# Kernel tuning notes

Hardware: AMD Instinct MI355X
Metric: run time of the kernel (lower is better)

Reference implementation:

```python
import jax, jax.numpy as jnp
import numpy as np

L, B, H, P = 2048, 32, 128, 256  # seq len, batch, feature dim, state dim


def setup_inputs() -> dict:
    key = jax.random.key(0)
    ks = jax.random.split(key, 9)
    log_min, log_max = np.log(0.001), np.log(0.1)
    return {
        "input_sequences": jax.random.normal(ks[0], (L, B, H), dtype=jnp.float32),
        # -Lambda.real of a HiPPO block diag is positive; emulate with small positive values
        "log_Lambda_real": jnp.log(0.5 + jax.random.uniform(ks[1], (P,), dtype=jnp.float32)),
        "Lambda_imag": jax.random.normal(ks[2], (P,), dtype=jnp.float32) * 3.0,
        "B_tilde_r": jax.random.normal(ks[3], (P, H), dtype=jnp.float32) * (0.5 / np.sqrt(H)),
        "B_tilde_i": jax.random.normal(ks[4], (P, H), dtype=jnp.float32) * (0.5 / np.sqrt(H)),
        "C_tilde_r": jax.random.normal(ks[5], (H, P), dtype=jnp.float32) * (0.5 / np.sqrt(P)),
        "C_tilde_i": jax.random.normal(ks[6], (H, P), dtype=jnp.float32) * (0.5 / np.sqrt(P)),
        "D": jax.random.normal(ks[7], (H,), dtype=jnp.float32),
        "log_Delta": log_min + (log_max - log_min) * jax.random.uniform(ks[8], (P,), dtype=jnp.float32),
    }


def reference(input_sequences, log_Lambda_real, Lambda_imag, B_tilde_r, B_tilde_i,
              C_tilde_r, C_tilde_i, D, log_Delta):
    l = input_sequences.shape[0]
    u = input_sequences.astype(jnp.complex64)  # (L,B,H)
    lam = (-jnp.exp(log_Lambda_real) + 1j * Lambda_imag).astype(jnp.complex64)  # (P,)
    log_Lambda_bar = lam * jnp.exp(log_Delta).astype(jnp.complex64)  # scale_factor=1.0
    # kernel[t, p] = exp(log_Lambda_bar[p] * (L-1-t))  -> (L,P)
    steps = jnp.arange(l - 1, -1, -1, dtype=jnp.float32).astype(jnp.complex64)
    kernel = jnp.exp(steps[:, None] * log_Lambda_bar[None, :])
    B_tilde = (B_tilde_r + 1j * B_tilde_i).astype(jnp.complex64)  # (P,H)
    B_bar = ((kernel[-2] - 1.0) / lam)[:, None] * B_tilde  # (P,H)
    Bu = jnp.einsum('nm,lbm->lbn', B_bar, u)  # (L,B,P)
    # FFT convolution: flipped kernel is exp(log_Lambda_bar * t)
    kff = jnp.fft.fft(kernel[::-1], n=2 * l, axis=0)[:, None, :]  # (2L,1,P)
    buff = jnp.fft.fft(Bu, n=2 * l, axis=0)  # (2L,B,P)
    o = jnp.fft.ifft(kff * buff, axis=0)[:l]  # (L,B,P)
    xs = jnp.einsum('hn,lbn->lbh', (C_tilde_r + 1j * C_tilde_i).astype(jnp.complex64), o)
    xs = xs + (D * input_sequences).astype(jnp.complex64)
    return jnp.real(xs)
```

## Files before the change

### kernel.cpp

```cpp
#include <hip/hip_runtime.h>
#include <math.h>

#define SL 2048
#define NB 32
#define NH 128
#define NP 256
#define NP2 512

typedef short bf16x8 __attribute__((ext_vector_type(8)));
typedef float f32x4  __attribute__((ext_vector_type(4)));

static __device__ __forceinline__ unsigned short f2bf(float x) {
    unsigned u = __float_as_uint(x);
    return (unsigned short)((u + 0x7fffu + ((u >> 16) & 1u)) >> 16);
}
static __device__ __forceinline__ float bf2f(unsigned short h) {
    return __uint_as_float(((unsigned)h) << 16);
}
static __device__ __forceinline__ void discretize(
    const float* __restrict__ logLr, const float* __restrict__ Lim,
    const float* __restrict__ logDt, int p, float& wr, float& wi)
{
    const float Lr = expf(logLr[p]);
    const float dt = expf(logDt[p]);
    const float ew = expf(-Lr * dt);
    const float ang = Lim[p] * dt;
    wr = ew * cosf(ang); wi = ew * sinf(ang);
}

__global__ __launch_bounds__(256) void k0(
    const float* __restrict__ logLr, const float* __restrict__ Lim,
    const float* __restrict__ logDt,
    const float* __restrict__ Br, const float* __restrict__ Bi,
    const float* __restrict__ Cr, const float* __restrict__ Ci,
    unsigned short* __restrict__ Bhat, unsigned short* __restrict__ Chat)
{
    const int tid = blockIdx.x * 256 + threadIdx.x;
    const int p = tid >> 7, h = tid & 127;
    float wr, wi; discretize(logLr, Lim, logDt, p, wr, wi);
    const float Lr = expf(logLr[p]), li = Lim[p];
    const float nr = wr - 1.0f, ni = wi;
    const float den = Lr * Lr + li * li;
    const float fr = (-nr * Lr + ni * li) / den;
    const float fi = (-ni * Lr - nr * li) / den;
    const float br = Br[p * NH + h], bi = Bi[p * NH + h];
    Bhat[(size_t)(2 * p)     * NH + h] = f2bf(fr * br - fi * bi);
    Bhat[(size_t)(2 * p + 1) * NH + h] = f2bf(fr * bi + fi * br);
    Chat[(size_t)h * NP2 + 2 * p]     = f2bf(Cr[h * NP + p]);
    Chat[(size_t)h * NP2 + 2 * p + 1] = f2bf(-Ci[h * NP + p]);
}

__global__ __launch_bounds__(256, 2) void gA(
    const float* __restrict__ u, const unsigned short* __restrict__ Bhat,
    const float* __restrict__ logLr, const float* __restrict__ Lim,
    const float* __restrict__ logDt,
    unsigned short* __restrict__ bu, float2* __restrict__ part)
{
    __shared__ unsigned short us[32][136];
    __shared__ unsigned xs[32 * 257];

    const int seg = blockIdx.x;
    const int b   = blockIdx.y;
    const int tid = threadIdx.x;
    const int wave = tid >> 6, lane = tid & 63;
    const int q = lane >> 4, c = lane & 15;
    const int pbase = wave * 128;

    bf16x8 A[4][8];
    #pragma unroll
    for (int kk = 0; kk < 4; ++kk)
        #pragma unroll
        for (int mt = 0; mt < 8; ++mt)
            A[kk][mt] = *(const bf16x8*)(Bhat + (size_t)(pbase + 16 * mt + c) * NH
                                              + kk * 32 + 8 * q);

    float wr, wi; discretize(logLr, Lim, logDt, tid, wr, wi);
    float W32r = wr, W32i = wi;
    #pragma unroll
    for (int t = 0; t < 5; ++t) { const float r = W32r * W32r - W32i * W32i;
                                  W32i = 2.f * W32r * W32i; W32r = r; }

    float2 pa = make_float2(0.f, 0.f);

    for (int t = 0; t < 4; ++t) {
        const int l0 = seg * 128 + t * 32;
        __syncthreads();
        {
            const int lrow = tid >> 3;
            const int hcol = (tid & 7) * 16;
            const float* up = u + (size_t)(l0 + lrow) * (NB * NH) + b * NH + hcol;
            float4 a = *(const float4*)(up + 0);
            float4 d = *(const float4*)(up + 4);
            float4 e = *(const float4*)(up + 8);
            float4 g = *(const float4*)(up + 12);
            uint4 w0, w1;
            w0.x = (unsigned)f2bf(a.x) | ((unsigned)f2bf(a.y) << 16);
            w0.y = (unsigned)f2bf(a.z) | ((unsigned)f2bf(a.w) << 16);
            w0.z = (unsigned)f2bf(d.x) | ((unsigned)f2bf(d.y) << 16);
            w0.w = (unsigned)f2bf(d.z) | ((unsigned)f2bf(d.w) << 16);
            w1.x = (unsigned)f2bf(e.x) | ((unsigned)f2bf(e.y) << 16);
            w1.y = (unsigned)f2bf(e.z) | ((unsigned)f2bf(e.w) << 16);
            w1.z = (unsigned)f2bf(g.x) | ((unsigned)f2bf(g.y) << 16);
            w1.w = (unsigned)f2bf(g.z) | ((unsigned)f2bf(g.w) << 16);
            *(uint4*)&us[lrow][hcol + 0] = w0;
            *(uint4*)&us[lrow][hcol + 8] = w1;
        }
        __syncthreads();

        f32x4 acc[8][2];
        #pragma unroll
        for (int mt = 0; mt < 8; ++mt)
            #pragma unroll
            for (int nt = 0; nt < 2; ++nt) acc[mt][nt] = (f32x4){0.f, 0.f, 0.f, 0.f};

        #pragma unroll
        for (int kk = 0; kk < 4; ++kk) {
            bf16x8 bfr[2];
            #pragma unroll
            for (int nt = 0; nt < 2; ++nt)
                bfr[nt] = *(const bf16x8*)&us[16 * nt + c][kk * 32 + 8 * q];
            #pragma unroll
            for (int mt = 0; mt < 8; ++mt)
                #pragma unroll
                for (int nt = 0; nt < 2; ++nt)
                    acc[mt][nt] = __builtin_amdgcn_mfma_f32_16x16x32_bf16(
                        A[kk][mt], bfr[nt], acc[mt][nt], 0, 0, 0);
        }

        #pragma unroll
        for (int mt = 0; mt < 8; ++mt)
            #pragma unroll
            for (int nt = 0; nt < 2; ++nt) {
                const int rw = 16 * nt + c;
                const int pp = pbase + 16 * mt + 4 * q;
                ushort4 st;
                st.x = f2bf(acc[mt][nt][0]); st.y = f2bf(acc[mt][nt][1]);
                st.z = f2bf(acc[mt][nt][2]); st.w = f2bf(acc[mt][nt][3]);
                *(ushort4*)(bu + ((size_t)(b * SL + l0 + rw)) * NP2 + pp) = st;
                const int col = (pp >> 1);
                xs[rw * 257 + col]     = (unsigned)st.x | ((unsigned)st.y << 16);
                xs[rw * 257 + col + 1] = (unsigned)st.z | ((unsigned)st.w << 16);
            }
        __syncthreads();

        {
            float sr = 0.f, si = 0.f;
            unsigned va[8], vb[8];
            #pragma unroll
            for (int j = 0; j < 8; ++j) va[j] = xs[j * 257 + tid];
            #pragma unroll
            for (int k8 = 0; k8 < 4; ++k8) {
                if (k8 < 3) {
                    #pragma unroll
                    for (int j = 0; j < 8; ++j) vb[j] = xs[((k8 + 1) * 8 + j) * 257 + tid];
                }
                #pragma unroll
                for (int j = 0; j < 8; ++j) {
                    const float xr = bf2f((unsigned short)(va[j] & 0xffffu));
                    const float xi = bf2f((unsigned short)(va[j] >> 16));
                    const float tr = wr * sr - wi * si + xr;
                    const float ti = wr * si + wi * sr + xi;
                    sr = tr; si = ti;
                }
                #pragma unroll
                for (int j = 0; j < 8; ++j) va[j] = vb[j];
            }
            if ((t & 1) == 0) {
                pa = make_float2(sr, si);
            } else {
                const float cr2 = W32r * pa.x - W32i * pa.y + sr;
                const float ci2 = W32r * pa.y + W32i * pa.x + si;
                part[((size_t)b * 32 + 2 * seg + (t >> 1)) * NP + tid] =
                    make_float2(cr2, ci2);
            }
        }
    }
}

__global__ __launch_bounds__(256) void s2(
    const float2* __restrict__ part, const float* __restrict__ logLr,
    const float* __restrict__ Lim, const float* __restrict__ logDt,
    float2* __restrict__ C)
{
    const int b = blockIdx.x, p = threadIdx.x;
    float wr, wi; discretize(logLr, Lim, logDt, p, wr, wi);
    float Wr = wr, Wi = wi;
    #pragma unroll
    for (int t = 0; t < 6; ++t) { const float r = Wr * Wr - Wi * Wi; Wi = 2.f * Wr * Wi; Wr = r; }
    float sr = 0.f, si = 0.f;
    for (int m = 0; m < 32; ++m) {
        C[(size_t)(b * 32 + m) * NP + p] = make_float2(sr, si);
        const float2 v = part[(size_t)(b * 32 + m) * NP + p];
        const float tr = Wr * sr - Wi * si + v.x;
        const float ti = Wr * si + Wi * sr + v.y;
        sr = tr; si = ti;
    }
}

__global__ __launch_bounds__(256, 2) void gB(
    const unsigned* __restrict__ bu32, const unsigned short* __restrict__ Chat,
    const float* __restrict__ logLr, const float* __restrict__ Lim,
    const float* __restrict__ logDt, const float2* __restrict__ C,
    const float* __restrict__ Dv, const float* __restrict__ u,
    float* __restrict__ out)
{
    __shared__ uint4 os4[4096];
    char*   osb  = (char*)os4;
    float2* carr = (float2*)os4;

    const int m = blockIdx.x, b = blockIdx.y;
    const int tid = threadIdx.x;
    const int w = tid >> 6, lane = tid & 63;
    const int p0 = lane * 4;

    float wr[4], wi[4];
    #pragma unroll
    for (int e = 0; e < 4; ++e) discretize(logLr, Lim, logDt, p0 + e, wr[e], wi[e]);

    float Wr[4], Wi[4];
    #pragma unroll
    for (int e = 0; e < 4; ++e) { Wr[e] = wr[e]; Wi[e] = wi[e]; }
    #pragma unroll
    for (int t = 0; t < 4; ++t)
        #pragma unroll
        for (int e = 0; e < 4; ++e) {
            const float r = Wr[e] * Wr[e] - Wi[e] * Wi[e];
            Wi[e] = 2.f * Wr[e] * Wi[e]; Wr[e] = r;
        }

    const unsigned* base = bu32 + ((size_t)(b * SL + m * 64 + w * 16)) * NP + p0;
    uint4 va[16];
    #pragma unroll
    for (int k = 0; k < 16; ++k) va[k] = *(const uint4*)(base + (size_t)k * NP);

    float sr[4] = {0.f, 0.f, 0.f, 0.f}, si[4] = {0.f, 0.f, 0.f, 0.f};
    #pragma unroll
    for (int k = 0; k < 16; ++k) {
        unsigned vv[4] = { va[k].x, va[k].y, va[k].z, va[k].w };
        #pragma unroll
        for (int e = 0; e < 4; ++e) {
            const float xr = bf2f((unsigned short)(vv[e] & 0xffffu));
            const float xi = bf2f((unsigned short)(vv[e] >> 16));
            const float tr = wr[e] * sr[e] - wi[e] * si[e] + xr;
            const float ti = wr[e] * si[e] + wi[e] * sr[e] + xi;
            sr[e] = tr; si[e] = ti;
        }
    }
    #pragma unroll
    for (int e = 0; e < 4; ++e) carr[w * NP + p0 + e] = make_float2(sr[e], si[e]);

    float Er[4], Ei[4];
    #pragma unroll
    for (int e = 0; e < 4; ++e) {
        const float2 E = C[((size_t)(b * 32 + m)) * NP + p0 + e];
        Er[e] = E.x; Ei[e] = E.y;
    }

    __syncthreads();
    float cjr[3][4], cji[3][4];
    #pragma unroll
    for (int j = 0; j < 3; ++j) if (j < w)
        #pragma unroll
        for (int e = 0; e < 4; ++e) {
            const float2 v = carr[j * NP + p0 + e];
            cjr[j][e] = v.x; cji[j][e] = v.y;
        }
    __syncthreads();

    #pragma unroll
    for (int j = 0; j < 3; ++j) if (j < w)
        #pragma unroll
        for (int e = 0; e < 4; ++e) {
            const float tr = Wr[e] * Er[e] - Wi[e] * Ei[e] + cjr[j][e];
            const float ti = Wr[e] * Ei[e] + Wi[e] * Er[e] + cji[j][e];
            Er[e] = tr; Ei[e] = ti;
        }

    #pragma unroll
    for (int e = 0; e < 4; ++e) { sr[e] = Er[e]; si[e] = Ei[e]; }
    #pragma unroll
    for (int k = 0; k < 16; ++k) {
        unsigned vv[4] = { va[k].x, va[k].y, va[k].z, va[k].w };
        unsigned ov[4];
        #pragma unroll
        for (int e = 0; e < 4; ++e) {
            const float xr = bf2f((unsigned short)(vv[e] & 0xffffu));
            const float xi = bf2f((unsigned short)(vv[e] >> 16));
            const float tr = wr[e] * sr[e] - wi[e] * si[e] + xr;
            const float ti = wr[e] * si[e] + wi[e] * sr[e] + xi;
            sr[e] = tr; si[e] = ti;
            ov[e] = (unsigned)f2bf(tr) | ((unsigned)f2bf(ti) << 16);
        }
        const int row = w * 16 + k;
        const unsigned byte = (((unsigned)row << 10) + ((unsigned)lane << 4))
                              ^ (((unsigned)(k & 7)) << 4);
        uint4 st = { ov[0], ov[1], ov[2], ov[3] };
        *(uint4*)(osb + byte) = st;
    }
    __syncthreads();

    const int q = lane >> 4, c = lane & 15;
    const int wm = w >> 1, wn = w & 1;
    const int hbase = wm * 64;
    const int lbase = m * 64 + wn * 32;

    f32x4 acc[4][2];
    #pragma unroll
    for (int mt = 0; mt < 4; ++mt)
        #pragma unroll
        for (int nt = 0; nt < 2; ++nt) acc[mt][nt] = (f32x4){0.f, 0.f, 0.f, 0.f};

    #pragma unroll 4
    for (int kk = 0; kk < 16; ++kk) {
        bf16x8 af[4];
        #pragma unroll
        for (int mt = 0; mt < 4; ++mt)
            af[mt] = *(const bf16x8*)(Chat + (size_t)(hbase + 16 * mt + c) * NP2
                                           + kk * 32 + 8 * q);
        bf16x8 bfr[2];
        #pragma unroll
        for (int nt = 0; nt < 2; ++nt) {
            const int r = wn * 32 + 16 * nt + c;
            const unsigned byte = (((unsigned)r << 10) + ((unsigned)kk << 6)
                                   + ((unsigned)q << 4))
                                  ^ (((unsigned)(c & 7)) << 4);
            bfr[nt] = *(const bf16x8*)(osb + byte);
        }
        #pragma unroll
        for (int mt = 0; mt < 4; ++mt)
            #pragma unroll
            for (int nt = 0; nt < 2; ++nt)
                acc[mt][nt] = __builtin_amdgcn_mfma_f32_16x16x32_bf16(
                    af[mt], bfr[nt], acc[mt][nt], 0, 0, 0);
    }

    #pragma unroll
    for (int mt = 0; mt < 4; ++mt) {
        const int h4 = hbase + 16 * mt + 4 * q;
        const float4 dd = *(const float4*)(Dv + h4);
        #pragma unroll
        for (int nt = 0; nt < 2; ++nt) {
            const int l = lbase + 16 * nt + c;
            const size_t off = ((size_t)l * NB + b) * NH + h4;
            const float4 uu = *(const float4*)(u + off);
            float4 ov;
            ov.x = acc[mt][nt][0] + dd.x * uu.x;
            ov.y = acc[mt][nt][1] + dd.y * uu.y;
            ov.z = acc[mt][nt][2] + dd.z * uu.z;
            ov.w = acc[mt][nt][3] + dd.w * uu.w;
            *(float4*)(out + off) = ov;
        }
    }
}

extern "C" void kernel_launch(void* const* d_in, const int* in_sizes, int n_in,
                              void* d_out, int out_size, void* d_ws, size_t ws_size,
                              hipStream_t stream)
{
    const float* u     = (const float*)d_in[0];
    const float* logLr = (const float*)d_in[1];
    const float* Lim   = (const float*)d_in[2];
    const float* Btr   = (const float*)d_in[3];
    const float* Bti   = (const float*)d_in[4];
    const float* Ctr   = (const float*)d_in[5];
    const float* Cti   = (const float*)d_in[6];
    const float* Dv    = (const float*)d_in[7];
    const float* logDt = (const float*)d_in[8];
    float* out = (float*)d_out;

    char* ws = (char*)d_ws;
    unsigned short* bu   = (unsigned short*)ws;
    float2*         part = (float2*)(ws + 67108864);
    float2*         Cst  = (float2*)(ws + 69206016);
    unsigned short* Bhat = (unsigned short*)(ws + 71303168);
    unsigned short* Chat = (unsigned short*)(ws + 71434240);

    k0<<<dim3((NP * NH) / 256), 256, 0, stream>>>(logLr, Lim, logDt,
                                                  Btr, Bti, Ctr, Cti, Bhat, Chat);
    gA<<<dim3(16, NB), 256, 0, stream>>>(u, Bhat, logLr, Lim, logDt, bu, part);
    s2<<<dim3(NB), 256, 0, stream>>>(part, logLr, Lim, logDt, Cst);
    gB<<<dim3(SL / 64, NB), 256, 0, stream>>>((const unsigned*)bu, Chat, logLr, Lim,
                                              logDt, Cst, Dv, u, out);
}
```

Before: 187.8 us.

## Split scan-fixup and output GEMM into separate kernels via global memory

The fused gB kernel is split in two. The first kernel finishes the chunked scan and writes the bf16 states back in place into the global bu buffer. The second kernel then reads those states from global memory as the MFMA B operand and does the C projection plus the D skip term. The aim is to drop the 64KB shared-memory staging, a barrier and the register pressure of the fused kernel, which should allow higher occupancy. The cost is an extra global write and read of the state tensor (about 64MB total) and a second kernel launch.

```diff
diff --git a/kernel.cpp b/kernel.cpp
--- a/kernel.cpp
+++ b/kernel.cpp
@@ -197,16 +197,12 @@
     }
 }
 
-__global__ __launch_bounds__(256, 2) void gB(
-    const unsigned* __restrict__ bu32, const unsigned short* __restrict__ Chat,
+__global__ __launch_bounds__(256) void sc(
+    unsigned* __restrict__ bu32,
     const float* __restrict__ logLr, const float* __restrict__ Lim,
-    const float* __restrict__ logDt, const float2* __restrict__ C,
-    const float* __restrict__ Dv, const float* __restrict__ u,
-    float* __restrict__ out)
-{
-    __shared__ uint4 os4[4096];
-    char*   osb  = (char*)os4;
-    float2* carr = (float2*)os4;
+    const float* __restrict__ logDt, const float2* __restrict__ C)
+{
+    __shared__ float2 carr[3 * NP];
 
     const int m = blockIdx.x, b = blockIdx.y;
     const int tid = threadIdx.x;
@@ -228,7 +224,7 @@
             Wi[e] = 2.f * Wr[e] * Wi[e]; Wr[e] = r;
         }
 
-    const unsigned* base = bu32 + ((size_t)(b * SL + m * 64 + w * 16)) * NP + p0;
+    unsigned* base = bu32 + ((size_t)(b * SL + m * 64 + w * 16)) * NP + p0;
     uint4 va[16];
     #pragma unroll
     for (int k = 0; k < 16; ++k) va[k] = *(const uint4*)(base + (size_t)k * NP);
@@ -246,8 +242,10 @@
             sr[e] = tr; si[e] = ti;
         }
     }
-    #pragma unroll
-    for (int e = 0; e < 4; ++e) carr[w * NP + p0 + e] = make_float2(sr[e], si[e]);
+    if (w < 3) {
+        #pragma unroll
+        for (int e = 0; e < 4; ++e) carr[w * NP + p0 + e] = make_float2(sr[e], si[e]);
+    }
 
     float Er[4], Ei[4];
     #pragma unroll
@@ -257,22 +255,14 @@
     }
 
     __syncthreads();
-    float cjr[3][4], cji[3][4];
+
     #pragma unroll
     for (int j = 0; j < 3; ++j) if (j < w)
         #pragma unroll
         for (int e = 0; e < 4; ++e) {
             const float2 v = carr[j * NP + p0 + e];
-            cjr[j][e] = v.x; cji[j][e] = v.y;
-        }
-    __syncthreads();
-
-    #pragma unroll
-    for (int j = 0; j < 3; ++j) if (j < w)
-        #pragma unroll
-        for (int e = 0; e < 4; ++e) {
-            const float tr = Wr[e] * Er[e] - Wi[e] * Ei[e] + cjr[j][e];
-            const float ti = Wr[e] * Ei[e] + Wi[e] * Er[e] + cji[j][e];
+            const float tr = Wr[e] * Er[e] - Wi[e] * Ei[e] + v.x;
+            const float ti = Wr[e] * Ei[e] + Wi[e] * Er[e] + v.y;
             Er[e] = tr; Ei[e] = ti;
         }
 
@@ -291,16 +281,21 @@
             sr[e] = tr; si[e] = ti;
             ov[e] = (unsigned)f2bf(tr) | ((unsigned)f2bf(ti) << 16);
         }
-        const int row = w * 16 + k;
-        const unsigned byte = (((unsigned)row << 10) + ((unsigned)lane << 4))
-                              ^ (((unsigned)(k & 7)) << 4);
         uint4 st = { ov[0], ov[1], ov[2], ov[3] };
-        *(uint4*)(osb + byte) = st;
-    }
-    __syncthreads();
-
+        *(uint4*)(base + (size_t)k * NP) = st;
+    }
+}
+
+__global__ __launch_bounds__(256) void g2(
+    const unsigned short* __restrict__ o, const unsigned short* __restrict__ Chat,
+    const float* __restrict__ Dv, const float* __restrict__ u,
+    float* __restrict__ out)
+{
+    const int m = blockIdx.x, b = blockIdx.y;
+    const int tid = threadIdx.x;
+    const int wave = tid >> 6, lane = tid & 63;
     const int q = lane >> 4, c = lane & 15;
-    const int wm = w >> 1, wn = w & 1;
+    const int wm = wave >> 1, wn = wave & 1;
     const int hbase = wm * 64;
     const int lbase = m * 64 + wn * 32;
 
@@ -319,13 +314,9 @@
                                            + kk * 32 + 8 * q);
         bf16x8 bfr[2];
         #pragma unroll
-        for (int nt = 0; nt < 2; ++nt) {
-            const int r = wn * 32 + 16 * nt + c;
-            const unsigned byte = (((unsigned)r << 10) + ((unsigned)kk << 6)
-                                   + ((unsigned)q << 4))
-                                  ^ (((unsigned)(c & 7)) << 4);
-            bfr[nt] = *(const bf16x8*)(osb + byte);
-        }
+        for (int nt = 0; nt < 2; ++nt)
+            bfr[nt] = *(const bf16x8*)(o + ((size_t)(b * SL + lbase + 16 * nt + c)) * NP2
+                                         + kk * 32 + 8 * q);
         #pragma unroll
         for (int mt = 0; mt < 4; ++mt)
             #pragma unroll
@@ -379,6 +370,6 @@
                                                   Btr, Bti, Ctr, Cti, Bhat, Chat);
     gA<<<dim3(16, NB), 256, 0, stream>>>(u, Bhat, logLr, Lim, logDt, bu, part);
     s2<<<dim3(NB), 256, 0, stream>>>(part, logLr, Lim, logDt, Cst);
-    gB<<<dim3(SL / 64, NB), 256, 0, stream>>>((const unsigned*)bu, Chat, logLr, Lim,
-                                              logDt, Cst, Dv, u, out);
-}
+    sc<<<dim3(SL / 64, NB), 256, 0, stream>>>((unsigned*)bu, logLr, Lim, logDt, Cst);
+    g2<<<dim3(SL / 64, NB), 256, 0, stream>>>(bu, Chat, Dv, u, out);
+}
```

Result: slower. 220.5 us (+17.4%).

## Split gB state dimension into two halves to raise occupancy and reblock Chat

Applied to the files above, without the earlier changes.

The gB kernel now handles the 256 state channels in two passes of 128. Each pass runs the chunked scan, fixes up the carries across waves, writes a half-width tile to shared memory and accumulates its share of the C-projection MFMAs. This shrinks the per-thread register array and the LDS tile, so launch bounds can be raised to 4 blocks per CU for better latency hiding. Chat is also stored blocked by k-tiles of 32 columns so that A-fragment loads are contiguous. In exchange there are extra barriers, the discretize setup runs twice, and the global loads per pass are narrower.

```diff
diff --git a/kernel.cpp b/kernel.cpp
--- a/kernel.cpp
+++ b/kernel.cpp
@@ -33,7 +33,7 @@
     const float* __restrict__ logDt,
     const float* __restrict__ Br, const float* __restrict__ Bi,
     const float* __restrict__ Cr, const float* __restrict__ Ci,
-    unsigned short* __restrict__ Bhat, unsigned short* __restrict__ Chat)
+    unsigned short* __restrict__ Bhat, unsigned short* __restrict__ ChatF)
 {
     const int tid = blockIdx.x * 256 + threadIdx.x;
     const int p = tid >> 7, h = tid & 127;
@@ -46,8 +46,9 @@
     const float br = Br[p * NH + h], bi = Bi[p * NH + h];
     Bhat[(size_t)(2 * p)     * NH + h] = f2bf(fr * br - fi * bi);
     Bhat[(size_t)(2 * p + 1) * NH + h] = f2bf(fr * bi + fi * br);
-    Chat[(size_t)h * NP2 + 2 * p]     = f2bf(Cr[h * NP + p]);
-    Chat[(size_t)h * NP2 + 2 * p + 1] = f2bf(-Ci[h * NP + p]);
+    const int col0 = 2 * p, col1 = 2 * p + 1;
+    ChatF[((size_t)(col0 >> 5) << 12) + (h << 5) + (col0 & 31)] = f2bf(Cr[h * NP + p]);
+    ChatF[((size_t)(col1 >> 5) << 12) + (h << 5) + (col1 & 31)] = f2bf(-Ci[h * NP + p]);
 }
 
 __global__ __launch_bounds__(256, 2) void gA(
@@ -197,108 +198,19 @@
     }
 }
 
-__global__ __launch_bounds__(256, 2) void gB(
-    const unsigned* __restrict__ bu32, const unsigned short* __restrict__ Chat,
+__global__ __launch_bounds__(256, 4) void gB(
+    const unsigned* __restrict__ bu32, const unsigned short* __restrict__ ChatF,
     const float* __restrict__ logLr, const float* __restrict__ Lim,
     const float* __restrict__ logDt, const float2* __restrict__ C,
     const float* __restrict__ Dv, const float* __restrict__ u,
     float* __restrict__ out)
 {
-    __shared__ uint4 os4[4096];
-    char*   osb  = (char*)os4;
-    float2* carr = (float2*)os4;
+    __shared__ char   osb[32768];
+    __shared__ float2 carr[2][3 * 128];
 
     const int m = blockIdx.x, b = blockIdx.y;
     const int tid = threadIdx.x;
     const int w = tid >> 6, lane = tid & 63;
-    const int p0 = lane * 4;
-
-    float wr[4], wi[4];
-    #pragma unroll
-    for (int e = 0; e < 4; ++e) discretize(logLr, Lim, logDt, p0 + e, wr[e], wi[e]);
-
-    float Wr[4], Wi[4];
-    #pragma unroll
-    for (int e = 0; e < 4; ++e) { Wr[e] = wr[e]; Wi[e] = wi[e]; }
-    #pragma unroll
-    for (int t = 0; t < 4; ++t)
-        #pragma unroll
-        for (int e = 0; e < 4; ++e) {
-            const float r = Wr[e] * Wr[e] - Wi[e] * Wi[e];
-            Wi[e] = 2.f * Wr[e] * Wi[e]; Wr[e] = r;
-        }
-
-    const unsigned* base = bu32 + ((size_t)(b * SL + m * 64 + w * 16)) * NP + p0;
-    uint4 va[16];
-    #pragma unroll
-    for (int k = 0; k < 16; ++k) va[k] = *(const uint4*)(base + (size_t)k * NP);
-
-    float sr[4] = {0.f, 0.f, 0.f, 0.f}, si[4] = {0.f, 0.f, 0.f, 0.f};
-    #pragma unroll
-    for (int k = 0; k < 16; ++k) {
-        unsigned vv[4] = { va[k].x, va[k].y, va[k].z, va[k].w };
-        #pragma unroll
-        for (int e = 0; e < 4; ++e) {
-            const float xr = bf2f((unsigned short)(vv[e] & 0xffffu));
-            const float xi = bf2f((unsigned short)(vv[e] >> 16));
-            const float tr = wr[e] * sr[e] - wi[e] * si[e] + xr;
-            const float ti = wr[e] * si[e] + wi[e] * sr[e] + xi;
-            sr[e] = tr; si[e] = ti;
-        }
-    }
-    #pragma unroll
-    for (int e = 0; e < 4; ++e) carr[w * NP + p0 + e] = make_float2(sr[e], si[e]);
-
-    float Er[4], Ei[4];
-    #pragma unroll
-    for (int e = 0; e < 4; ++e) {
-        const float2 E = C[((size_t)(b * 32 + m)) * NP + p0 + e];
-        Er[e] = E.x; Ei[e] = E.y;
-    }
-
-    __syncthreads();
-    float cjr[3][4], cji[3][4];
-    #pragma unroll
-    for (int j = 0; j < 3; ++j) if (j < w)
-        #pragma unroll
-        for (int e = 0; e < 4; ++e) {
-            const float2 v = carr[j * NP + p0 + e];
-            cjr[j][e] = v.x; cji[j][e] = v.y;
-        }
-    __syncthreads();
-
-    #pragma unroll
-    for (int j = 0; j < 3; ++j) if (j < w)
-        #pragma unroll
-        for (int e = 0; e < 4; ++e) {
-            const float tr = Wr[e] * Er[e] - Wi[e] * Ei[e] + cjr[j][e];
-            const float ti = Wr[e] * Ei[e] + Wi[e] * Er[e] + cji[j][e];
-            Er[e] = tr; Ei[e] = ti;
-        }
-
-    #pragma unroll
-    for (int e = 0; e < 4; ++e) { sr[e] = Er[e]; si[e] = Ei[e]; }
-    #pragma unroll
-    for (int k = 0; k < 16; ++k) {
-        unsigned vv[4] = { va[k].x, va[k].y, va[k].z, va[k].w };
-        unsigned ov[4];
-        #pragma unroll
-        for (int e = 0; e < 4; ++e) {
-            const float xr = bf2f((unsigned short)(vv[e] & 0xffffu));
-            const float xi = bf2f((unsigned short)(vv[e] >> 16));
-            const float tr = wr[e] * sr[e] - wi[e] * si[e] + xr;
-            const float ti = wr[e] * si[e] + wi[e] * sr[e] + xi;
-            sr[e] = tr; si[e] = ti;
-            ov[e] = (unsigned)f2bf(tr) | ((unsigned)f2bf(ti) << 16);
-        }
-        const int row = w * 16 + k;
-        const unsigned byte = (((unsigned)row << 10) + ((unsigned)lane << 4))
-                              ^ (((unsigned)(k & 7)) << 4);
-        uint4 st = { ov[0], ov[1], ov[2], ov[3] };
-        *(uint4*)(osb + byte) = st;
-    }
-    __syncthreads();
-
     const int q = lane >> 4, c = lane & 15;
     const int wm = w >> 1, wn = w & 1;
     const int hbase = wm * 64;
@@ -310,28 +222,117 @@
         #pragma unroll
         for (int nt = 0; nt < 2; ++nt) acc[mt][nt] = (f32x4){0.f, 0.f, 0.f, 0.f};
 
-    #pragma unroll 4
-    for (int kk = 0; kk < 16; ++kk) {
-        bf16x8 af[4];
-        #pragma unroll
-        for (int mt = 0; mt < 4; ++mt)
-            af[mt] = *(const bf16x8*)(Chat + (size_t)(hbase + 16 * mt + c) * NP2
-                                           + kk * 32 + 8 * q);
-        bf16x8 bfr[2];
-        #pragma unroll
-        for (int nt = 0; nt < 2; ++nt) {
-            const int r = wn * 32 + 16 * nt + c;
-            const unsigned byte = (((unsigned)r << 10) + ((unsigned)kk << 6)
-                                   + ((unsigned)q << 4))
-                                  ^ (((unsigned)(c & 7)) << 4);
-            bfr[nt] = *(const bf16x8*)(osb + byte);
-        }
-        #pragma unroll
-        for (int mt = 0; mt < 4; ++mt)
-            #pragma unroll
-            for (int nt = 0; nt < 2; ++nt)
-                acc[mt][nt] = __builtin_amdgcn_mfma_f32_16x16x32_bf16(
-                    af[mt], bfr[nt], acc[mt][nt], 0, 0, 0);
+    #pragma unroll 1
+    for (int half = 0; half < 2; ++half) {
+        const int pc0 = half * 128 + lane * 2;
+
+        float wr[2], wi[2];
+        #pragma unroll
+        for (int e = 0; e < 2; ++e) discretize(logLr, Lim, logDt, pc0 + e, wr[e], wi[e]);
+
+        float Wr[2], Wi[2];
+        #pragma unroll
+        for (int e = 0; e < 2; ++e) { Wr[e] = wr[e]; Wi[e] = wi[e]; }
+        #pragma unroll
+        for (int t = 0; t < 4; ++t)
+            #pragma unroll
+            for (int e = 0; e < 2; ++e) {
+                const float r = Wr[e] * Wr[e] - Wi[e] * Wi[e];
+                Wi[e] = 2.f * Wr[e] * Wi[e]; Wr[e] = r;
+            }
+
+        const unsigned* base = bu32 + ((size_t)(b * SL + m * 64 + w * 16)) * NP
+                                    + half * 128 + lane * 2;
+        uint2 va[16];
+        #pragma unroll
+        for (int k = 0; k < 16; ++k) va[k] = *(const uint2*)(base + (size_t)k * NP);
+
+        float sr[2] = {0.f, 0.f}, si[2] = {0.f, 0.f};
+        #pragma unroll
+        for (int k = 0; k < 16; ++k) {
+            unsigned vv[2] = { va[k].x, va[k].y };
+            #pragma unroll
+            for (int e = 0; e < 2; ++e) {
+                const float xr = bf2f((unsigned short)(vv[e] & 0xffffu));
+                const float xi = bf2f((unsigned short)(vv[e] >> 16));
+                const float tr = wr[e] * sr[e] - wi[e] * si[e] + xr;
+                const float ti = wr[e] * si[e] + wi[e] * sr[e] + xi;
+                sr[e] = tr; si[e] = ti;
+            }
+        }
+        if (w < 3) {
+            #pragma unroll
+            for (int e = 0; e < 2; ++e)
+                carr[half][w * 128 + lane * 2 + e] = make_float2(sr[e], si[e]);
+        }
+
+        float Er[2], Ei[2];
+        #pragma unroll
+        for (int e = 0; e < 2; ++e) {
+            const float2 E = C[((size_t)(b * 32 + m)) * NP + pc0 + e];
+            Er[e] = E.x; Ei[e] = E.y;
+        }
+
+        __syncthreads();
+
+        #pragma unroll
+        for (int j = 0; j < 3; ++j) if (j < w)
+            #pragma unroll
+            for (int e = 0; e < 2; ++e) {
+                const float2 v = carr[half][j * 128 + lane * 2 + e];
+                const float tr = Wr[e] * Er[e] - Wi[e] * Ei[e] + v.x;
+                const float ti = Wr[e] * Ei[e] + Wi[e] * Er[e] + v.y;
+                Er[e] = tr; Ei[e] = ti;
+            }
+
+        #pragma unroll
+        for (int e = 0; e < 2; ++e) { sr[e] = Er[e]; si[e] = Ei[e]; }
+        #pragma unroll
+        for (int k = 0; k < 16; ++k) {
+            unsigned vv[2] = { va[k].x, va[k].y };
+            unsigned ov[2];
+            #pragma unroll
+            for (int e = 0; e < 2; ++e) {
+                const float xr = bf2f((unsigned short)(vv[e] & 0xffffu));
+                const float xi = bf2f((unsigned short)(vv[e] >> 16));
+                const float tr = wr[e] * sr[e] - wi[e] * si[e] + xr;
+                const float ti = wr[e] * si[e] + wi[e] * sr[e] + xi;
+                sr[e] = tr; si[e] = ti;
+                ov[e] = (unsigned)f2bf(tr) | ((unsigned)f2bf(ti) << 16);
+            }
+            const int row = w * 16 + k;
+            const unsigned byte = (((unsigned)row << 9) + ((unsigned)lane << 3))
+                                  ^ (((unsigned)(row & 7)) << 4);
+            uint2 st = { ov[0], ov[1] };
+            *(uint2*)(osb + byte) = st;
+        }
+        __syncthreads();
+
+        #pragma unroll 4
+        for (int kl = 0; kl < 8; ++kl) {
+            const int kk = half * 8 + kl;
+            bf16x8 af[4];
+            #pragma unroll
+            for (int mt = 0; mt < 4; ++mt)
+                af[mt] = *(const bf16x8*)(ChatF + ((size_t)kk << 12)
+                                          + ((hbase + (mt << 4) + c) << 5) + (q << 3));
+            bf16x8 bfr[2];
+            #pragma unroll
+            for (int nt = 0; nt < 2; ++nt) {
+                const int r = wn * 32 + 16 * nt + c;
+                const unsigned byte = (((unsigned)r << 9) + ((unsigned)kl << 6)
+                                       + ((unsigned)q << 4))
+                                      ^ (((unsigned)(c & 7)) << 4);
+                bfr[nt] = *(const bf16x8*)(osb + byte);
+            }
+            #pragma unroll
+            for (int mt = 0; mt < 4; ++mt)
+                #pragma unroll
+                for (int nt = 0; nt < 2; ++nt)
+                    acc[mt][nt] = __builtin_amdgcn_mfma_f32_16x16x32_bf16(
+                        af[mt], bfr[nt], acc[mt][nt], 0, 0, 0);
+        }
+        if (half == 0) __syncthreads();
     }
 
     #pragma unroll
```

New measurement: 176.2 us. 6.2% less time.
